# Performance work log

Measured on AMD Instinct MI355X. Metric: run time of the kernel, lower is better.

## Reference

```python
import jax, jax.numpy as jnp
from jax import lax
import numpy as np

BATCH, DIM, HID, NSTEPS = 32768, 128, 256, 50

def setup_inputs() -> dict:
    key = jax.random.key(0)
    k1, k2, k3 = jax.random.split(key, 3)
    inputs = jax.random.normal(k1, (BATCH, DIM), dtype=jnp.float32)
    # increasing timestamps over [0, 1] -> 50 Euler steps of dt = 0.02
    timestamps = jnp.linspace(0.0, 1.0, NSTEPS + 1, dtype=jnp.float32)
    # small init keeps the Euler trajectory stable
    W1 = jax.random.normal(k2, (DIM, HID), dtype=jnp.float32) * 0.05
    b1 = jnp.zeros((HID,), dtype=jnp.float32)
    W2 = jax.random.normal(k3, (HID, DIM), dtype=jnp.float32) * 0.05
    b2 = jnp.zeros((DIM,), dtype=jnp.float32)
    return {"inputs": inputs, "timestamps": timestamps, "W1": W1, "b1": b1, "W2": W2, "b2": b2}

def reference(inputs, timestamps, W1, b1, W2, b2):
    """Euler integration of dh/dt = f(h) = tanh(h@W1+b1)@W2+b2; returns final state h(T).
    Matches AdjointODEFunc.forward (which returns states[-1])."""
    dts = timestamps[1:] - timestamps[:-1]  # [NSTEPS]

    def f(h):  # vector field (time-invariant MLP)
        return jnp.tanh(h @ W1 + b1) @ W2 + b2

    def step(h, dt):
        return h + dt * f(h), None

    h_final, _ = lax.scan(step, inputs, dts)
    return h_final
```

## Files before the change

kernel.cpp:

```cpp
#include <hip/hip_runtime.h>


typedef __attribute__((ext_vector_type(8))) short short8;
typedef __attribute__((ext_vector_type(4))) float float4v;
typedef __attribute__((ext_vector_type(4))) int int4v;

union FB { int4v i; short8 s; };

#define W1F_OFF 0
#define W2F_OFF 65536
#define B1_OFF  131072
#define DT_OFF  132096
#define LDS_BYTES 132352

#define TSCALE 2.8853900817779268f

__device__ __forceinline__ unsigned rne2(float x) {
  unsigned u = __float_as_uint(x);
  return u + 0x7fffu + ((u >> 16) & 1u);
}

#if __has_builtin(__builtin_amdgcn_cvt_pk_bf16_f32)
__device__ __forceinline__ int pk2(float lo, float hi) {
  return __builtin_bit_cast(int, __builtin_amdgcn_cvt_pk_bf16_f32(lo, hi));
}
#else
__device__ __forceinline__ int pk2(float lo, float hi) {
  return (int)__builtin_amdgcn_perm(rne2(hi), rne2(lo), 0x07060302u);
}
#endif

__device__ __forceinline__ int4v packfrag(float4v e, float4v o) {
  int4v f;
  f.x = pk2(e.x, e.y);
  f.y = pk2(e.z, e.w);
  f.z = pk2(o.x, o.y);
  f.w = pk2(o.z, o.w);
  return f;
}

#define MFMA16(a, b, c) __builtin_amdgcn_mfma_f32_16x16x32_bf16(a, b, c, 0, 0, 0)

extern "C" __global__ __launch_bounds__(512, 2)
void ode_kernel(const float* __restrict__ inp, const float* __restrict__ ts,
                const float* __restrict__ W1, const float* __restrict__ b1,
                const float* __restrict__ W2, const float* __restrict__ b2,
                float* __restrict__ out) {
  __shared__ __align__(16) char ldsb[LDS_BYTES];
  float* b1f = (float*)(ldsb + B1_OFF);
  float* dtf = (float*)(ldsb + DT_OFF);

  const int tid = threadIdx.x;
  const int lane = tid & 63, wave = tid >> 6;
  const int ln = lane & 15;
  const int q = lane >> 4;
  const int row = blockIdx.x * 128 + wave * 16 + ln;

  #pragma unroll 1
  for (int it = 0; it < 8; it++) {
    const int pi = it * 512 + tid;
    const int fid = pi >> 6, L = pi & 63;
    const int nt = fid >> 2, c = fid & 3;
    const int lf = L & 15, qf = L >> 4;
    const int n = nt * 16 + lf;
    const int kb = c * 32 + qf * 4;
    float v0 = W1[(kb + 0) * 256 + n] * TSCALE;
    float v1 = W1[(kb + 1) * 256 + n] * TSCALE;
    float v2 = W1[(kb + 2) * 256 + n] * TSCALE;
    float v3 = W1[(kb + 3) * 256 + n] * TSCALE;
    float v4 = W1[(kb + 16) * 256 + n] * TSCALE;
    float v5 = W1[(kb + 17) * 256 + n] * TSCALE;
    float v6 = W1[(kb + 18) * 256 + n] * TSCALE;
    float v7 = W1[(kb + 19) * 256 + n] * TSCALE;
    int4v d = {pk2(v0, v1), pk2(v2, v3), pk2(v4, v5), pk2(v6, v7)};
    *(int4v*)(ldsb + W1F_OFF + pi * 16) = d;
  }
  #pragma unroll 1
  for (int it = 0; it < 8; it++) {
    const int pi = it * 512 + tid;
    const int fid = pi >> 6, L = pi & 63;
    const int p = fid >> 3, tb = fid & 7;
    const int lf = L & 15, qf = L >> 4;
    const int d_out = tb * 16 + lf;
    const int kb = p * 32 + qf * 4;
    float v0 = W2[(kb + 0) * 128 + d_out];
    float v1 = W2[(kb + 1) * 128 + d_out];
    float v2 = W2[(kb + 2) * 128 + d_out];
    float v3 = W2[(kb + 3) * 128 + d_out];
    float v4 = W2[(kb + 16) * 128 + d_out];
    float v5 = W2[(kb + 17) * 128 + d_out];
    float v6 = W2[(kb + 18) * 128 + d_out];
    float v7 = W2[(kb + 19) * 128 + d_out];
    int4v d = {pk2(v0, v1), pk2(v2, v3), pk2(v4, v5), pk2(v6, v7)};
    *(int4v*)(ldsb + W2F_OFF + pi * 16) = d;
  }
  if (tid < 256) b1f[tid] = b1[tid] * TSCALE;
  if (tid < 50) dtf[tid] = ts[tid + 1] - ts[tid];

  float4v b2v[8];
  #pragma unroll
  for (int tb = 0; tb < 8; tb++)
    b2v[tb] = *(const float4v*)&b2[tb * 16 + q * 4];

  float4v h4[8];
  #pragma unroll
  for (int tb = 0; tb < 8; tb++)
    h4[tb] = *(const float4v*)&inp[row * 128 + tb * 16 + q * 4];

  __syncthreads();

  const int4v* w1f = (const int4v*)(ldsb + W1F_OFF) + lane;
  const int4v* w2f = (const int4v*)(ldsb + W2F_OFF) + lane;

  #pragma unroll 1
  for (int s = 0; s < 50; s++) {
    const float dt = dtf[s];
    const float m2dt = -2.0f * dt;

    FB hb[4];
    #pragma unroll
    for (int kc = 0; kc < 4; kc++)
      hb[kc].i = packfrag(h4[2 * kc], h4[2 * kc + 1]);

    FB af;
    {
      FB wA[4], wB[4];
      #pragma unroll
      for (int c = 0; c < 4; c++) {
        wA[c].i = w1f[(0 * 4 + c) * 64];
        wB[c].i = w1f[(1 * 4 + c) * 64];
      }
      float4v g0 = *(const float4v*)&b1f[0 * 16 + q * 4];
      float4v g1 = *(const float4v*)&b1f[1 * 16 + q * 4];
      #pragma unroll
      for (int c = 0; c < 4; c++) {
        g0 = MFMA16(wA[c].s, hb[c].s, g0);
        g1 = MFMA16(wB[c].s, hb[c].s, g1);
      }
      float4v a0, a1;
      #pragma unroll
      for (int r = 0; r < 4; r++) {
        a0[r] = fmaf(__builtin_amdgcn_rcpf(__builtin_amdgcn_exp2f(g0[r]) + 1.0f), m2dt, dt);
        a1[r] = fmaf(__builtin_amdgcn_rcpf(__builtin_amdgcn_exp2f(g1[r]) + 1.0f), m2dt, dt);
      }
      af.i = packfrag(a0, a1);
    }

    #pragma unroll 1
    for (int p = 1; p < 8; p++) {
      const int nt0 = 2 * p, nt1 = 2 * p + 1;
      FB wA[4], wB[4];
      #pragma unroll
      for (int c = 0; c < 4; c++) {
        wA[c].i = w1f[(nt0 * 4 + c) * 64];
        wB[c].i = w1f[(nt1 * 4 + c) * 64];
      }
      float4v g0 = *(const float4v*)&b1f[nt0 * 16 + q * 4];
      float4v g1 = *(const float4v*)&b1f[nt1 * 16 + q * 4];
      #pragma unroll
      for (int c = 0; c < 4; c++) {
        g0 = MFMA16(wA[c].s, hb[c].s, g0);
        g1 = MFMA16(wB[c].s, hb[c].s, g1);
      }
      {
        FB w2r[8];
        #pragma unroll
        for (int tb = 0; tb < 8; tb++)
          w2r[tb].i = w2f[((p - 1) * 8 + tb) * 64];
        #pragma unroll
        for (int tb = 0; tb < 8; tb++)
          h4[tb] = MFMA16(w2r[tb].s, af.s, h4[tb]);
      }
      float4v a0, a1;
      #pragma unroll
      for (int r = 0; r < 4; r++) {
        a0[r] = fmaf(__builtin_amdgcn_rcpf(__builtin_amdgcn_exp2f(g0[r]) + 1.0f), m2dt, dt);
        a1[r] = fmaf(__builtin_amdgcn_rcpf(__builtin_amdgcn_exp2f(g1[r]) + 1.0f), m2dt, dt);
      }
      af.i = packfrag(a0, a1);
    }

    {
      FB w2r[8];
      #pragma unroll
      for (int tb = 0; tb < 8; tb++)
        w2r[tb].i = w2f[(7 * 8 + tb) * 64];
      #pragma unroll
      for (int tb = 0; tb < 8; tb++)
        h4[tb] = MFMA16(w2r[tb].s, af.s, h4[tb]);
    }

    #pragma unroll
    for (int tb = 0; tb < 8; tb++)
      #pragma unroll
      for (int r = 0; r < 4; r++)
        h4[tb][r] = fmaf(dt, b2v[tb][r], h4[tb][r]);
  }

  #pragma unroll
  for (int tb = 0; tb < 8; tb++)
    *(float4v*)&out[row * 128 + tb * 16 + q * 4] = h4[tb];
}

extern "C" void kernel_launch(void* const* d_in, const int* in_sizes, int n_in,
                              void* d_out, int out_size, void* d_ws, size_t ws_size,
                              hipStream_t stream) {
  const float* inp = (const float*)d_in[0];
  const float* ts  = (const float*)d_in[1];
  const float* W1  = (const float*)d_in[2];
  const float* b1  = (const float*)d_in[3];
  const float* W2  = (const float*)d_in[4];
  const float* b2  = (const float*)d_in[5];
  hipLaunchKernelGGL(ode_kernel, dim3(256), dim3(512), 0, stream,
                     inp, ts, W1, b1, W2, b2, (float*)d_out);
}
```

Before: 310.4 us.

## Process two 16-row tiles per wave to reuse LDS weight fragments

Each wave now carries two independent 16-row state tiles, so every W1/W2 fragment loaded from LDS feeds two MFMAs instead of one. Blocks shrink to 256 threads while still covering 128 rows each, halving LDS weight traffic per row and giving independent MFMA chains to interleave. The cost is roughly double the register footprint per thread and half as many waves per CU, which lowers occupancy and the ability to hide latency.

```diff
diff --git a/kernel.cpp b/kernel.cpp
--- a/kernel.cpp
+++ b/kernel.cpp
@@ -41,7 +41,7 @@
 
 #define MFMA16(a, b, c) __builtin_amdgcn_mfma_f32_16x16x32_bf16(a, b, c, 0, 0, 0)
 
-extern "C" __global__ __launch_bounds__(512, 2)
+extern "C" __global__ __launch_bounds__(256, 1)
 void ode_kernel(const float* __restrict__ inp, const float* __restrict__ ts,
                 const float* __restrict__ W1, const float* __restrict__ b1,
                 const float* __restrict__ W2, const float* __restrict__ b2,
@@ -54,11 +54,12 @@
   const int lane = tid & 63, wave = tid >> 6;
   const int ln = lane & 15;
   const int q = lane >> 4;
-  const int row = blockIdx.x * 128 + wave * 16 + ln;
+  const int rowa = blockIdx.x * 128 + wave * 32 + ln;
+  const int rowb = rowa + 16;
 
   #pragma unroll 1
-  for (int it = 0; it < 8; it++) {
-    const int pi = it * 512 + tid;
+  for (int it = 0; it < 16; it++) {
+    const int pi = it * 256 + tid;
     const int fid = pi >> 6, L = pi & 63;
     const int nt = fid >> 2, c = fid & 3;
     const int lf = L & 15, qf = L >> 4;
@@ -76,8 +77,8 @@
     *(int4v*)(ldsb + W1F_OFF + pi * 16) = d;
   }
   #pragma unroll 1
-  for (int it = 0; it < 8; it++) {
-    const int pi = it * 512 + tid;
+  for (int it = 0; it < 16; it++) {
+    const int pi = it * 256 + tid;
     const int fid = pi >> 6, L = pi & 63;
     const int p = fid >> 3, tb = fid & 7;
     const int lf = L & 15, qf = L >> 4;
@@ -94,7 +95,7 @@
     int4v d = {pk2(v0, v1), pk2(v2, v3), pk2(v4, v5), pk2(v6, v7)};
     *(int4v*)(ldsb + W2F_OFF + pi * 16) = d;
   }
-  if (tid < 256) b1f[tid] = b1[tid] * TSCALE;
+  b1f[tid] = b1[tid] * TSCALE;
   if (tid < 50) dtf[tid] = ts[tid + 1] - ts[tid];
 
   float4v b2v[8];
@@ -102,10 +103,12 @@
   for (int tb = 0; tb < 8; tb++)
     b2v[tb] = *(const float4v*)&b2[tb * 16 + q * 4];
 
-  float4v h4[8];
+  float4v h4a[8], h4b[8];
   #pragma unroll
-  for (int tb = 0; tb < 8; tb++)
-    h4[tb] = *(const float4v*)&inp[row * 128 + tb * 16 + q * 4];
+  for (int tb = 0; tb < 8; tb++) {
+    h4a[tb] = *(const float4v*)&inp[rowa * 128 + tb * 16 + q * 4];
+    h4b[tb] = *(const float4v*)&inp[rowb * 128 + tb * 16 + q * 4];
+  }
 
   __syncthreads();
 
@@ -117,12 +120,14 @@
     const float dt = dtf[s];
     const float m2dt = -2.0f * dt;
 
-    FB hb[4];
+    FB hba[4], hbb[4];
     #pragma unroll
-    for (int kc = 0; kc < 4; kc++)
-      hb[kc].i = packfrag(h4[2 * kc], h4[2 * kc + 1]);
-
-    FB af;
+    for (int kc = 0; kc < 4; kc++) {
+      hba[kc].i = packfrag(h4a[2 * kc], h4a[2 * kc + 1]);
+      hbb[kc].i = packfrag(h4b[2 * kc], h4b[2 * kc + 1]);
+    }
+
+    FB afa, afb;
     {
       FB wA[4], wB[4];
       #pragma unroll
@@ -130,20 +135,26 @@
         wA[c].i = w1f[(0 * 4 + c) * 64];
         wB[c].i = w1f[(1 * 4 + c) * 64];
       }
-      float4v g0 = *(const float4v*)&b1f[0 * 16 + q * 4];
-      float4v g1 = *(const float4v*)&b1f[1 * 16 + q * 4];
-      #pragma unroll
-      for (int c = 0; c < 4; c++) {
-        g0 = MFMA16(wA[c].s, hb[c].s, g0);
-        g1 = MFMA16(wB[c].s, hb[c].s, g1);
-      }
-      float4v a0, a1;
+      const float4v bi0 = *(const float4v*)&b1f[0 * 16 + q * 4];
+      const float4v bi1 = *(const float4v*)&b1f[1 * 16 + q * 4];
+      float4v g0a = bi0, g1a = bi1, g0b = bi0, g1b = bi1;
+      #pragma unroll
+      for (int c = 0; c < 4; c++) {
+        g0a = MFMA16(wA[c].s, hba[c].s, g0a);
+        g1a = MFMA16(wB[c].s, hba[c].s, g1a);
+        g0b = MFMA16(wA[c].s, hbb[c].s, g0b);
+        g1b = MFMA16(wB[c].s, hbb[c].s, g1b);
+      }
+      float4v a0a, a1a, a0b, a1b;
       #pragma unroll
       for (int r = 0; r < 4; r++) {
-        a0[r] = fmaf(__builtin_amdgcn_rcpf(__builtin_amdgcn_exp2f(g0[r]) + 1.0f), m2dt, dt);
-        a1[r] = fmaf(__builtin_amdgcn_rcpf(__builtin_amdgcn_exp2f(g1[r]) + 1.0f), m2dt, dt);
-      }
-      af.i = packfrag(a0, a1);
+        a0a[r] = fmaf(__builtin_amdgcn_rcpf(__builtin_amdgcn_exp2f(g0a[r]) + 1.0f), m2dt, dt);
+        a1a[r] = fmaf(__builtin_amdgcn_rcpf(__builtin_amdgcn_exp2f(g1a[r]) + 1.0f), m2dt, dt);
+        a0b[r] = fmaf(__builtin_amdgcn_rcpf(__builtin_amdgcn_exp2f(g0b[r]) + 1.0f), m2dt, dt);
+        a1b[r] = fmaf(__builtin_amdgcn_rcpf(__builtin_amdgcn_exp2f(g1b[r]) + 1.0f), m2dt, dt);
+      }
+      afa.i = packfrag(a0a, a1a);
+      afb.i = packfrag(a0b, a1b);
     }
 
     #pragma unroll 1
@@ -155,29 +166,36 @@
         wA[c].i = w1f[(nt0 * 4 + c) * 64];
         wB[c].i = w1f[(nt1 * 4 + c) * 64];
       }
-      float4v g0 = *(const float4v*)&b1f[nt0 * 16 + q * 4];
-      float4v g1 = *(const float4v*)&b1f[nt1 * 16 + q * 4];
-      #pragma unroll
-      for (int c = 0; c < 4; c++) {
-        g0 = MFMA16(wA[c].s, hb[c].s, g0);
-        g1 = MFMA16(wB[c].s, hb[c].s, g1);
-      }
-      {
-        FB w2r[8];
-        #pragma unroll
-        for (int tb = 0; tb < 8; tb++)
-          w2r[tb].i = w2f[((p - 1) * 8 + tb) * 64];
-        #pragma unroll
-        for (int tb = 0; tb < 8; tb++)
-          h4[tb] = MFMA16(w2r[tb].s, af.s, h4[tb]);
-      }
-      float4v a0, a1;
+      FB w2r[8];
+      #pragma unroll
+      for (int tb = 0; tb < 8; tb++)
+        w2r[tb].i = w2f[((p - 1) * 8 + tb) * 64];
+
+      const float4v bi0 = *(const float4v*)&b1f[nt0 * 16 + q * 4];
+      const float4v bi1 = *(const float4v*)&b1f[nt1 * 16 + q * 4];
+      float4v g0a = bi0, g1a = bi1, g0b = bi0, g1b = bi1;
+      #pragma unroll
+      for (int c = 0; c < 4; c++) {
+        g0a = MFMA16(wA[c].s, hba[c].s, g0a);
+        g1a = MFMA16(wB[c].s, hba[c].s, g1a);
+        g0b = MFMA16(wA[c].s, hbb[c].s, g0b);
+        g1b = MFMA16(wB[c].s, hbb[c].s, g1b);
+      }
+      #pragma unroll
+      for (int tb = 0; tb < 8; tb++) {
+        h4a[tb] = MFMA16(w2r[tb].s, afa.s, h4a[tb]);
+        h4b[tb] = MFMA16(w2r[tb].s, afb.s, h4b[tb]);
+      }
+      float4v a0a, a1a, a0b, a1b;
       #pragma unroll
       for (int r = 0; r < 4; r++) {
-        a0[r] = fmaf(__builtin_amdgcn_rcpf(__builtin_amdgcn_exp2f(g0[r]) + 1.0f), m2dt, dt);
-        a1[r] = fmaf(__builtin_amdgcn_rcpf(__builtin_amdgcn_exp2f(g1[r]) + 1.0f), m2dt, dt);
-      }
-      af.i = packfrag(a0, a1);
+        a0a[r] = fmaf(__builtin_amdgcn_rcpf(__builtin_amdgcn_exp2f(g0a[r]) + 1.0f), m2dt, dt);
+        a1a[r] = fmaf(__builtin_amdgcn_rcpf(__builtin_amdgcn_exp2f(g1a[r]) + 1.0f), m2dt, dt);
+        a0b[r] = fmaf(__builtin_amdgcn_rcpf(__builtin_amdgcn_exp2f(g0b[r]) + 1.0f), m2dt, dt);
+        a1b[r] = fmaf(__builtin_amdgcn_rcpf(__builtin_amdgcn_exp2f(g1b[r]) + 1.0f), m2dt, dt);
+      }
+      afa.i = packfrag(a0a, a1a);
+      afb.i = packfrag(a0b, a1b);
     }
 
     {
@@ -186,20 +204,26 @@
       for (int tb = 0; tb < 8; tb++)
         w2r[tb].i = w2f[(7 * 8 + tb) * 64];
       #pragma unroll
-      for (int tb = 0; tb < 8; tb++)
-        h4[tb] = MFMA16(w2r[tb].s, af.s, h4[tb]);
+      for (int tb = 0; tb < 8; tb++) {
+        h4a[tb] = MFMA16(w2r[tb].s, afa.s, h4a[tb]);
+        h4b[tb] = MFMA16(w2r[tb].s, afb.s, h4b[tb]);
+      }
     }
 
     #pragma unroll
     for (int tb = 0; tb < 8; tb++)
       #pragma unroll
-      for (int r = 0; r < 4; r++)
-        h4[tb][r] = fmaf(dt, b2v[tb][r], h4[tb][r]);
+      for (int r = 0; r < 4; r++) {
+        h4a[tb][r] = fmaf(dt, b2v[tb][r], h4a[tb][r]);
+        h4b[tb][r] = fmaf(dt, b2v[tb][r], h4b[tb][r]);
+      }
   }
 
   #pragma unroll
-  for (int tb = 0; tb < 8; tb++)
-    *(float4v*)&out[row * 128 + tb * 16 + q * 4] = h4[tb];
+  for (int tb = 0; tb < 8; tb++) {
+    *(float4v*)&out[rowa * 128 + tb * 16 + q * 4] = h4a[tb];
+    *(float4v*)&out[rowb * 128 + tb * 16 + q * 4] = h4b[tb];
+  }
 }
 
 extern "C" void kernel_launch(void* const* d_in, const int* in_sizes, int n_in,
@@ -211,6 +235,6 @@
   const float* b1  = (const float*)d_in[3];
   const float* W2  = (const float*)d_in[4];
   const float* b2  = (const float*)d_in[5];
-  hipLaunchKernelGGL(ode_kernel, dim3(256), dim3(512), 0, stream,
+  hipLaunchKernelGGL(ode_kernel, dim3(256), dim3(256), 0, stream,
                      inp, ts, W1, b1, W2, b2, (float*)d_out);
 }
```

New measurement: 406.2 us. +30.9%, slower.
